# Kernel optimization log

Measured on AMD Instinct MI355X. Metric: run time of the kernel, lower is better.

Reference implementation:

```python
import jax, jax.numpy as jnp
from jax import lax
import numpy as np

NUM_DROPS = 10
MIN_R, MAX_R = 60.0, 80.0
BETA = 1.8
# fixed (non-trainable) blur radii from the module buffer
BLUR_RADII = [11.3535, 17.9381, 5.7966, 10.8586, 5.5301, 15.9075, 12.3225, 13.4871, 6.6639, 9.5413]

def _ksize(r):
    k = int(2 * r) + 1
    return k + 1 if k % 2 == 0 else k

KSIZES = [_ksize(r) for r in BLUR_RADII]  # [23, 37, 13, 23, 13, 33, 25, 27, 15, 21]

# learned-parameter initial values from the module source
POS0 = np.array([[0.07, -0.68], [-0.83, -0.12], [0.57, -0.09], [-0.12, -0.19],
                 [-0.47, -0.12], [0.83, -0.45], [0.42, -0.62], [-0.31, -0.66],
                 [-0.71, -0.64], [0.2, -0.14]], dtype=np.float32)
RAD0 = np.array([68.9755, 66.3124, 78.3028, 64.0275, 64.5939,
                 64.1804, 61.6286, 73.2401, 66.8596, 59.9934], dtype=np.float32)


def _gaussian_blur(x, sigma, ksize):
    # torchvision GaussianBlur: separable depthwise conv, reflect padding
    half = (ksize - 1) * 0.5
    xs = jnp.linspace(-half, half, ksize)
    pdf = jnp.exp(-0.5 * (xs / sigma) ** 2)
    k1 = (pdf / pdf.sum()).astype(x.dtype)
    pad = ksize // 2
    C = x.shape[1]
    dn = ('NCHW', 'OIHW', 'NCHW')
    kv = jnp.tile(k1.reshape(1, 1, ksize, 1), (C, 1, 1, 1))
    kh = jnp.tile(k1.reshape(1, 1, 1, ksize), (C, 1, 1, 1))
    xp = jnp.pad(x, ((0, 0), (0, 0), (pad, pad), (0, 0)), mode='reflect')
    x = lax.conv_general_dilated(xp, kv, (1, 1), 'VALID', dimension_numbers=dn, feature_group_count=C)
    xp = jnp.pad(x, ((0, 0), (0, 0), (0, 0), (pad, pad)), mode='reflect')
    x = lax.conv_general_dilated(xp, kh, (1, 1), 'VALID', dimension_numbers=dn, feature_group_count=C)
    return x


def setup_inputs() -> dict:
    key = jax.random.key(0)
    img = jax.random.uniform(key, (16, 3, 768, 768), dtype=jnp.float32)
    positions = jnp.asarray(POS0)
    radius = jnp.asarray(RAD0)
    return {"img": img, "positions": positions, "radius": radius}


def reference(img, positions, radius):
    B, C, H, W = img.shape
    pos = jnp.clip(positions, -1.0, 1.0)
    rad = jnp.clip(radius, MIN_R, MAX_R)
    hv = jnp.arange(H, dtype=img.dtype)[:, None]  # [H,1]
    wv = jnp.arange(W, dtype=img.dtype)[None, :]  # [1,W]
    out = img
    # drops are identical across the batch, so process whole batch per drop
    for j in range(NUM_DROPS):
        x0 = (pos[j, 0] + 1.0) / 2.0 * W
        y0 = (pos[j, 1] + 1.0) / 2.0 * H
        wr = rad[j]
        hr = wr * 0.8
        d = (hv - y0) ** 2 / hr ** 2 + (wv - x0) ** 2 / wr ** 2  # [H,W]
        mask = jnp.clip(jnp.exp(-(d ** BETA) + 1e-10), 0.0, 1.0)
        blurred = _gaussian_blur(out * mask[None, None], BLUR_RADII[j], KSIZES[j])
        out = blurred * mask[None, None] + out * (1.0 - mask[None, None])
    return out
```

## Files before the change

### kernel.cpp

```cpp
#include <hip/hip_runtime.h>
#include <cmath>

namespace {

constexpr int B = 16, C = 3, H = 768, W = 768;
constexpr int HW = H * W;
constexpr int BC = B * C;
constexpr int NDROPS = 10;
constexpr int KS[NDROPS] = {23, 37, 13, 23, 13, 33, 25, 27, 15, 21};
constexpr float BLUR_R[NDROPS] = {11.3535f, 17.9381f, 5.7966f, 10.8586f, 5.5301f,
                                  15.9075f, 12.3225f, 13.4871f, 6.6639f, 9.5413f};
constexpr int MAXK = 37;
constexpr int MAXP = MAXK / 2;

constexpr float SFAC = 2.17f;
constexpr int BOXW = 384;
constexpr int BOXH = 288;
constexpr int VW = 448;
constexpr int YT = 16;

struct TapW {
    float w[MAXK];
};

}

__device__ inline int refl(int v, int n) {
    return v < 0 ? -v : (v >= n ? 2 * n - 2 - v : v);
}

__device__ inline void drop_box(const float* __restrict__ pos,
                                const float* __restrict__ rad, int j,
                                int& bx0, int& by0) {
    float px = fminf(fmaxf(pos[2 * j + 0], -1.f), 1.f);
    float py = fminf(fmaxf(pos[2 * j + 1], -1.f), 1.f);
    float wr = fminf(fmaxf(rad[j], 60.f), 80.f);
    float x0 = (px + 1.f) * 0.5f * (float)W;
    float y0 = (py + 1.f) * 0.5f * (float)H;
    float hr = wr * 0.8f;
    bx0 = max(0, (int)floorf(x0 - SFAC * wr));
    by0 = max(0, (int)floorf(y0 - SFAC * hr));
}

__global__ void mask_kernel(const float* __restrict__ pos,
                            const float* __restrict__ rad,
                            float* __restrict__ masks) {
    int idx = blockIdx.x * blockDim.x + threadIdx.x;
    if (idx >= HW) return;
    int y = idx / W;
    int x = idx - y * W;
    float fy = (float)y;
    float fx = (float)x;
#pragma unroll
    for (int j = 0; j < NDROPS; ++j) {
        float px = fminf(fmaxf(pos[2 * j + 0], -1.f), 1.f);
        float py = fminf(fmaxf(pos[2 * j + 1], -1.f), 1.f);
        float wr = fminf(fmaxf(rad[j], 60.f), 80.f);
        float x0 = (px + 1.f) * 0.5f * (float)W;
        float y0 = (py + 1.f) * 0.5f * (float)H;
        float hr = wr * 0.8f;
        float dy = fy - y0;
        float dx = fx - x0;
        float d = dy * dy / (hr * hr) + dx * dx / (wr * wr);
        float m = expf(-powf(d, 1.8f) + 1e-10f);
        m = fminf(fmaxf(m, 0.f), 1.f);
        masks[j * HW + idx] = m;
    }
}

__global__ void copy_kernel(const float4* __restrict__ src,
                            float4* __restrict__ dst, int n) {
    int i = blockIdx.x * blockDim.x + threadIdx.x;
    if (i < n) dst[i] = src[i];
}

template <int K>
__global__ __launch_bounds__(256) void fusedV(
    const float* __restrict__ out, const float* __restrict__ mask,
    float* __restrict__ vtmp, const float* __restrict__ pos,
    const float* __restrict__ rad, int j, TapW tw) {
    constexpr int P = K / 2;
    constexpr int TR = YT + K - 1;
    __shared__ float prod[TR][64];

    int bx0, by0;
    drop_box(pos, rad, j, bx0, by0);
    int c = blockIdx.x * 64 + threadIdx.x;
    int yi0 = blockIdx.y * YT;
    int bc = blockIdx.z;
    int rx = refl(bx0 - MAXP + c, W);
    const float* op = out + (size_t)bc * HW;

    for (int lr = threadIdx.y; lr < TR; lr += 4) {
        int ry = refl(by0 + yi0 - P + lr, H);
        int off = ry * W + rx;
        prod[lr][threadIdx.x] = op[off] * mask[off];
    }
    __syncthreads();

    float acc[4] = {0.f, 0.f, 0.f, 0.f};
    int base = threadIdx.y * 4;
#pragma unroll
    for (int t = 0; t < K + 3; ++t) {
        float v = prod[base + t][threadIdx.x];
#pragma unroll
        for (int o = 0; o < 4; ++o) {
            int ti = t - o;
            if (ti >= 0 && ti < K) acc[o] += tw.w[ti] * v;
        }
    }
    float* vp = vtmp + ((size_t)bc * BOXH + yi0 + base) * VW + c;
#pragma unroll
    for (int o = 0; o < 4; ++o) vp[(size_t)o * VW] = acc[o];
}

template <int K>
__global__ __launch_bounds__(256) void blurH2(
    const float* __restrict__ vtmp, const float* __restrict__ mask,
    float* __restrict__ out, const float* __restrict__ pos,
    const float* __restrict__ rad, int j, TapW tw) {
    constexpr int P = K / 2;
    constexpr int OFF = MAXP - P;
    int bx0, by0;
    drop_box(pos, rad, j, bx0, by0);
    int c = blockIdx.x * 64 + threadIdx.x;
    int yi = blockIdx.y * 4 + threadIdx.y;
    int bc = blockIdx.z;
    int x = bx0 + c;
    int y = by0 + yi;
    if (x >= W || y >= H) return;
    const float* vrow = vtmp + ((size_t)bc * BOXH + yi) * VW + (c + OFF);
    float sum = 0.f;
#pragma unroll
    for (int t = 0; t < K; ++t) sum += tw.w[t] * vrow[t];
    float m = mask[y * W + x];
    size_t idx = (size_t)bc * HW + (size_t)y * W + x;
    out[idx] = sum * m + out[idx] * (1.f - m);
}

static void make_weights(int j, TapW& tw) {
    int K = KS[j];
    float sigma = BLUR_R[j];
    float half = (K - 1) * 0.5f;
    float sum = 0.f;
    for (int i = 0; i < K; ++i) {
        float xx = -half + (float)i;
        float v = xx / sigma;
        float p = expf(-0.5f * v * v);
        tw.w[i] = p;
        sum += p;
    }
    for (int i = 0; i < K; ++i) tw.w[i] /= sum;
    for (int i = K; i < MAXK; ++i) tw.w[i] = 0.f;
}

template <int K>
static void launch_pair(hipStream_t stream, const float* mask, float* vtmp,
                        float* out, const float* pos, const float* rad, int j,
                        const TapW& tw) {
    dim3 blk(64, 4, 1);
    dim3 gV(VW / 64, BOXH / YT, BC);
    dim3 gH(BOXW / 64, BOXH / 4, BC);
    fusedV<K><<<gV, blk, 0, stream>>>(out, mask, vtmp, pos, rad, j, tw);
    blurH2<K><<<gH, blk, 0, stream>>>(vtmp, mask, out, pos, rad, j, tw);
}

static void launch_drop(int K, hipStream_t stream, const float* mask,
                        float* vtmp, float* out, const float* pos,
                        const float* rad, int j, const TapW& tw) {
    switch (K) {
        case 13: launch_pair<13>(stream, mask, vtmp, out, pos, rad, j, tw); break;
        case 15: launch_pair<15>(stream, mask, vtmp, out, pos, rad, j, tw); break;
        case 21: launch_pair<21>(stream, mask, vtmp, out, pos, rad, j, tw); break;
        case 23: launch_pair<23>(stream, mask, vtmp, out, pos, rad, j, tw); break;
        case 25: launch_pair<25>(stream, mask, vtmp, out, pos, rad, j, tw); break;
        case 27: launch_pair<27>(stream, mask, vtmp, out, pos, rad, j, tw); break;
        case 33: launch_pair<33>(stream, mask, vtmp, out, pos, rad, j, tw); break;
        case 37: launch_pair<37>(stream, mask, vtmp, out, pos, rad, j, tw); break;
    }
}

extern "C" void kernel_launch(void* const* d_in, const int* in_sizes, int n_in,
                              void* d_out, int out_size, void* d_ws,
                              size_t ws_size, hipStream_t stream) {
    const float* img = (const float*)d_in[0];
    const float* pos = (const float*)d_in[1];
    const float* rad = (const float*)d_in[2];
    float* out = (float*)d_out;

    float* masks = (float*)d_ws;
    float* vtmp = masks + (size_t)NDROPS * HW;

    mask_kernel<<<(HW + 255) / 256, 256, 0, stream>>>(pos, rad, masks);
    copy_kernel<<<(BC * HW / 4 + 255) / 256, 256, 0, stream>>>(
        (const float4*)img, (float4*)out, BC * HW / 4);

    for (int j = 0; j < NDROPS; ++j) {
        TapW tw;
        make_weights(j, tw);
        launch_drop(KS[j], stream, masks + (size_t)j * HW, vtmp, out, pos, rad,
                    j, tw);
    }
}
```

Measured before the change: 640.2 us.

## Fuse vertical and horizontal blur in shared memory with box-local masks

```diff
diff --git a/kernel.cpp b/kernel.cpp
--- a/kernel.cpp
+++ b/kernel.cpp
@@ -16,8 +16,9 @@
 constexpr float SFAC = 2.17f;
 constexpr int BOXW = 384;
 constexpr int BOXH = 288;
-constexpr int VW = 448;
-constexpr int YT = 16;
+constexpr int YT = 32;
+constexpr int MH = BOXH + 2 * MAXP;
+constexpr int MW = 448;
 
 struct TapW {
     float w[MAXK];
@@ -29,43 +30,46 @@
     return v < 0 ? -v : (v >= n ? 2 * n - 2 - v : v);
 }
 
+__device__ inline void drop_params(const float* __restrict__ pos,
+                                   const float* __restrict__ rad, int j,
+                                   float& x0, float& y0, float& wr, float& hr) {
+    float px = fminf(fmaxf(pos[2 * j + 0], -1.f), 1.f);
+    float py = fminf(fmaxf(pos[2 * j + 1], -1.f), 1.f);
+    wr = fminf(fmaxf(rad[j], 60.f), 80.f);
+    x0 = (px + 1.f) * 0.5f * (float)W;
+    y0 = (py + 1.f) * 0.5f * (float)H;
+    hr = wr * 0.8f;
+}
+
 __device__ inline void drop_box(const float* __restrict__ pos,
                                 const float* __restrict__ rad, int j,
                                 int& bx0, int& by0) {
-    float px = fminf(fmaxf(pos[2 * j + 0], -1.f), 1.f);
-    float py = fminf(fmaxf(pos[2 * j + 1], -1.f), 1.f);
-    float wr = fminf(fmaxf(rad[j], 60.f), 80.f);
-    float x0 = (px + 1.f) * 0.5f * (float)W;
-    float y0 = (py + 1.f) * 0.5f * (float)H;
-    float hr = wr * 0.8f;
+    float x0, y0, wr, hr;
+    drop_params(pos, rad, j, x0, y0, wr, hr);
     bx0 = max(0, (int)floorf(x0 - SFAC * wr));
     by0 = max(0, (int)floorf(y0 - SFAC * hr));
 }
 
-__global__ void mask_kernel(const float* __restrict__ pos,
-                            const float* __restrict__ rad,
-                            float* __restrict__ masks) {
-    int idx = blockIdx.x * blockDim.x + threadIdx.x;
-    if (idx >= HW) return;
-    int y = idx / W;
-    int x = idx - y * W;
-    float fy = (float)y;
-    float fx = (float)x;
-#pragma unroll
-    for (int j = 0; j < NDROPS; ++j) {
-        float px = fminf(fmaxf(pos[2 * j + 0], -1.f), 1.f);
-        float py = fminf(fmaxf(pos[2 * j + 1], -1.f), 1.f);
-        float wr = fminf(fmaxf(rad[j], 60.f), 80.f);
-        float x0 = (px + 1.f) * 0.5f * (float)W;
-        float y0 = (py + 1.f) * 0.5f * (float)H;
-        float hr = wr * 0.8f;
-        float dy = fy - y0;
-        float dx = fx - x0;
-        float d = dy * dy / (hr * hr) + dx * dx / (wr * wr);
-        float m = expf(-powf(d, 1.8f) + 1e-10f);
-        m = fminf(fmaxf(m, 0.f), 1.f);
-        masks[j * HW + idx] = m;
-    }
+__global__ void maskbox_kernel(const float* __restrict__ pos,
+                               const float* __restrict__ rad,
+                               float* __restrict__ mbox) {
+    int j = blockIdx.y;
+    int idx = blockIdx.x * 256 + threadIdx.x;
+    if (idx >= MH * MW) return;
+    int yi = idx / MW;
+    int xi = idx - yi * MW;
+    int bx0, by0;
+    drop_box(pos, rad, j, bx0, by0);
+    float x0, y0, wr, hr;
+    drop_params(pos, rad, j, x0, y0, wr, hr);
+    int rx = refl(bx0 - MAXP + xi, W);
+    int ry = refl(by0 - MAXP + yi, H);
+    float dy = (float)ry - y0;
+    float dx = (float)rx - x0;
+    float d = dy * dy / (hr * hr) + dx * dx / (wr * wr);
+    float m = expf(-powf(d, 1.8f) + 1e-10f);
+    m = fminf(fmaxf(m, 0.f), 1.f);
+    mbox[(size_t)j * MH * MW + idx] = m;
 }
 
 __global__ void copy_kernel(const float4* __restrict__ src,
@@ -75,67 +79,100 @@
 }
 
 template <int K>
-__global__ __launch_bounds__(256) void fusedV(
-    const float* __restrict__ out, const float* __restrict__ mask,
-    float* __restrict__ vtmp, const float* __restrict__ pos,
+__global__ __launch_bounds__(256) void fusedDrop(
+    const float* __restrict__ out, const float* __restrict__ mbox,
+    float* __restrict__ stage, const float* __restrict__ pos,
     const float* __restrict__ rad, int j, TapW tw) {
     constexpr int P = K / 2;
+    constexpr int TC = 64 + K - 1;
     constexpr int TR = YT + K - 1;
-    __shared__ float prod[TR][64];
+    constexpr int PC = TC + 2;
+    constexpr int VC = TC + 1;
+    __shared__ float prod[TR][PC];
+    __shared__ float vbl[YT][VC];
 
     int bx0, by0;
     drop_box(pos, rad, j, bx0, by0);
-    int c = blockIdx.x * 64 + threadIdx.x;
-    int yi0 = blockIdx.y * YT;
+    int tx = threadIdx.x, ty = threadIdx.y;
+    int xb = blockIdx.x * 64;
+    int yb = blockIdx.y * YT;
     int bc = blockIdx.z;
-    int rx = refl(bx0 - MAXP + c, W);
+    const float* mb = mbox + (size_t)j * MH * MW;
     const float* op = out + (size_t)bc * HW;
 
-    for (int lr = threadIdx.y; lr < TR; lr += 4) {
-        int ry = refl(by0 + yi0 - P + lr, H);
-        int off = ry * W + rx;
-        prod[lr][threadIdx.x] = op[off] * mask[off];
+    for (int cc = tx; cc < TC; cc += 64) {
+        int rx = refl(bx0 + xb - P + cc, W);
+        int xim = xb + cc + (MAXP - P);
+        for (int r = ty; r < TR; r += 4) {
+            int ry = refl(by0 + yb - P + r, H);
+            prod[r][cc] = op[ry * W + rx] * mb[(yb + r + (MAXP - P)) * MW + xim];
+        }
     }
     __syncthreads();
 
-    float acc[4] = {0.f, 0.f, 0.f, 0.f};
-    int base = threadIdx.y * 4;
-#pragma unroll
-    for (int t = 0; t < K + 3; ++t) {
-        float v = prod[base + t][threadIdx.x];
-#pragma unroll
-        for (int o = 0; o < 4; ++o) {
-            int ti = t - o;
-            if (ti >= 0 && ti < K) acc[o] += tw.w[ti] * v;
+    {
+        int c0 = 2 * tx;
+        int base = ty * 8;
+        if (c0 < TC) {
+            float a0[8] = {0, 0, 0, 0, 0, 0, 0, 0};
+            float a1[8] = {0, 0, 0, 0, 0, 0, 0, 0};
+#pragma unroll
+            for (int t = 0; t < K + 7; ++t) {
+                float2 v = *(const float2*)&prod[base + t][c0];
+#pragma unroll
+                for (int o = 0; o < 8; ++o) {
+                    int ti = t - o;
+                    if (ti >= 0 && ti < K) {
+                        a0[o] += tw.w[ti] * v.x;
+                        a1[o] += tw.w[ti] * v.y;
+                    }
+                }
+            }
+#pragma unroll
+            for (int o = 0; o < 8; ++o) {
+                vbl[base + o][c0] = a0[o];
+                vbl[base + o][c0 + 1] = a1[o];
+            }
         }
     }
-    float* vp = vtmp + ((size_t)bc * BOXH + yi0 + base) * VW + c;
-#pragma unroll
-    for (int o = 0; o < 4; ++o) vp[(size_t)o * VW] = acc[o];
-}
-
-template <int K>
-__global__ __launch_bounds__(256) void blurH2(
-    const float* __restrict__ vtmp, const float* __restrict__ mask,
+    __syncthreads();
+
+    {
+        int tid = ty * 64 + tx;
+        int xq = (tid & 7) * 8;
+        int yi = tid >> 3;
+        float acc[8] = {0, 0, 0, 0, 0, 0, 0, 0};
+#pragma unroll
+        for (int t = 0; t < K + 7; ++t) {
+            float v = vbl[yi][xq + t];
+#pragma unroll
+            for (int o = 0; o < 8; ++o) {
+                int ti = t - o;
+                if (ti >= 0 && ti < K) acc[o] += tw.w[ti] * v;
+            }
+        }
+        float* srow = stage + ((size_t)bc * BOXH + (yb + yi)) * BOXW + (xb + xq);
+        *(float4*)&srow[0] = make_float4(acc[0], acc[1], acc[2], acc[3]);
+        *(float4*)&srow[4] = make_float4(acc[4], acc[5], acc[6], acc[7]);
+    }
+}
+
+__global__ __launch_bounds__(256) void composite_kernel(
+    const float* __restrict__ stage, const float* __restrict__ mbox,
     float* __restrict__ out, const float* __restrict__ pos,
-    const float* __restrict__ rad, int j, TapW tw) {
-    constexpr int P = K / 2;
-    constexpr int OFF = MAXP - P;
+    const float* __restrict__ rad, int j) {
     int bx0, by0;
     drop_box(pos, rad, j, bx0, by0);
-    int c = blockIdx.x * 64 + threadIdx.x;
+    int ci = blockIdx.x * 64 + threadIdx.x;
     int yi = blockIdx.y * 4 + threadIdx.y;
     int bc = blockIdx.z;
-    int x = bx0 + c;
+    int x = bx0 + ci;
     int y = by0 + yi;
     if (x >= W || y >= H) return;
-    const float* vrow = vtmp + ((size_t)bc * BOXH + yi) * VW + (c + OFF);
-    float sum = 0.f;
-#pragma unroll
-    for (int t = 0; t < K; ++t) sum += tw.w[t] * vrow[t];
-    float m = mask[y * W + x];
-    size_t idx = (size_t)bc * HW + (size_t)y * W + x;
-    out[idx] = sum * m + out[idx] * (1.f - m);
+    float m = mbox[(size_t)j * MH * MW + (size_t)(yi + MAXP) * MW + (ci + MAXP)];
+    float s = stage[((size_t)bc * BOXH + yi) * BOXW + ci];
+    size_t o = (size_t)bc * HW + (size_t)y * W + x;
+    out[o] = s * m + out[o] * (1.f - m);
 }
 
 static void make_weights(int j, TapW& tw) {
@@ -155,29 +192,30 @@
 }
 
 template <int K>
-static void launch_pair(hipStream_t stream, const float* mask, float* vtmp,
-                        float* out, const float* pos, const float* rad, int j,
-                        const TapW& tw) {
+static void launch_fused(hipStream_t stream, const float* out,
+                         const float* mbox, float* stage, const float* pos,
+                         const float* rad, int j, const TapW& tw) {
     dim3 blk(64, 4, 1);
-    dim3 gV(VW / 64, BOXH / YT, BC);
-    dim3 gH(BOXW / 64, BOXH / 4, BC);
-    fusedV<K><<<gV, blk, 0, stream>>>(out, mask, vtmp, pos, rad, j, tw);
-    blurH2<K><<<gH, blk, 0, stream>>>(vtmp, mask, out, pos, rad, j, tw);
-}
-
-static void launch_drop(int K, hipStream_t stream, const float* mask,
-                        float* vtmp, float* out, const float* pos,
+    dim3 grid(BOXW / 64, BOXH / YT, BC);
+    fusedDrop<K><<<grid, blk, 0, stream>>>(out, mbox, stage, pos, rad, j, tw);
+}
+
+static void launch_drop(int K, hipStream_t stream, float* out,
+                        const float* mbox, float* stage, const float* pos,
                         const float* rad, int j, const TapW& tw) {
     switch (K) {
-        case 13: launch_pair<13>(stream, mask, vtmp, out, pos, rad, j, tw); break;
-        case 15: launch_pair<15>(stream, mask, vtmp, out, pos, rad, j, tw); break;
-        case 21: launch_pair<21>(stream, mask, vtmp, out, pos, rad, j, tw); break;
-        case 23: launch_pair<23>(stream, mask, vtmp, out, pos, rad, j, tw); break;
-        case 25: launch_pair<25>(stream, mask, vtmp, out, pos, rad, j, tw); break;
-        case 27: launch_pair<27>(stream, mask, vtmp, out, pos, rad, j, tw); break;
-        case 33: launch_pair<33>(stream, mask, vtmp, out, pos, rad, j, tw); break;
-        case 37: launch_pair<37>(stream, mask, vtmp, out, pos, rad, j, tw); break;
-    }
+        case 13: launch_fused<13>(stream, out, mbox, stage, pos, rad, j, tw); break;
+        case 15: launch_fused<15>(stream, out, mbox, stage, pos, rad, j, tw); break;
+        case 21: launch_fused<21>(stream, out, mbox, stage, pos, rad, j, tw); break;
+        case 23: launch_fused<23>(stream, out, mbox, stage, pos, rad, j, tw); break;
+        case 25: launch_fused<25>(stream, out, mbox, stage, pos, rad, j, tw); break;
+        case 27: launch_fused<27>(stream, out, mbox, stage, pos, rad, j, tw); break;
+        case 33: launch_fused<33>(stream, out, mbox, stage, pos, rad, j, tw); break;
+        case 37: launch_fused<37>(stream, out, mbox, stage, pos, rad, j, tw); break;
+    }
+    dim3 blk(64, 4, 1);
+    dim3 grid(BOXW / 64, BOXH / 4, BC);
+    composite_kernel<<<grid, blk, 0, stream>>>(stage, mbox, out, pos, rad, j);
 }
 
 extern "C" void kernel_launch(void* const* d_in, const int* in_sizes, int n_in,
@@ -188,17 +226,17 @@
     const float* rad = (const float*)d_in[2];
     float* out = (float*)d_out;
 
-    float* masks = (float*)d_ws;
-    float* vtmp = masks + (size_t)NDROPS * HW;
-
-    mask_kernel<<<(HW + 255) / 256, 256, 0, stream>>>(pos, rad, masks);
+    float* mbox = (float*)d_ws;
+    float* stage = mbox + (size_t)NDROPS * MH * MW;
+
+    maskbox_kernel<<<dim3((MH * MW + 255) / 256, NDROPS), 256, 0, stream>>>(
+        pos, rad, mbox);
     copy_kernel<<<(BC * HW / 4 + 255) / 256, 256, 0, stream>>>(
         (const float4*)img, (float4*)out, BC * HW / 4);
 
     for (int j = 0; j < NDROPS; ++j) {
         TapW tw;
         make_weights(j, tw);
-        launch_drop(KS[j], stream, masks + (size_t)j * HW, vtmp, out, pos, rad,
-                    j, tw);
-    }
-}
+        launch_drop(KS[j], stream, out, mbox, stage, pos, rad, j, tw);
+    }
+}
```

New measurement: 690.1 us. +7.8%, slower.
